# Kernel optimization log

Hardware: AMD Instinct MI355X
Metric: run time of the kernel (lower is better)

## Reference

```python
import jax, jax.numpy as jnp
import numpy as np

NUM_GRAPHS = 512  # static number of segments (graphs in the batch)
EPS = 1e-05


def setup_inputs() -> dict:
    key = jax.random.key(0)
    k1, k2 = jax.random.split(key)
    N, C = 500000, 128
    x = jax.random.normal(k1, (N, C), dtype=jnp.float32)
    batch = jnp.sort(jax.random.randint(k2, (N,), 0, NUM_GRAPHS)).astype(jnp.int64)
    weight = jnp.ones((C,), dtype=jnp.float32)
    bias = jnp.zeros((C,), dtype=jnp.float32)
    return {"x": x, "batch": batch, "weight": weight, "bias": bias}


def reference(x, batch, weight, bias):
    # Per-graph mean/var over nodes (dim=0 within each graph), per channel.
    seg = batch.astype(jnp.int32)
    counts = jax.ops.segment_sum(jnp.ones((x.shape[0],), x.dtype), seg,
                                 num_segments=NUM_GRAPHS)  # [B]
    counts = jnp.maximum(counts, 1.0)[:, None]             # guard empty graphs
    sums = jax.ops.segment_sum(x, seg, num_segments=NUM_GRAPHS)          # [B, C]
    sqsums = jax.ops.segment_sum(x * x, seg, num_segments=NUM_GRAPHS)    # [B, C]
    mean = sums / counts                                   # [B, C]
    var = sqsums / counts - mean * mean                    # biased (unbiased=False)
    inv_std = jax.lax.rsqrt(var + EPS)
    out = (x - mean[seg]) * inv_std[seg]                   # gather per node
    return out * weight + bias
```

## Files before the change

### kernel.cpp

```cpp
#include <hip/hip_runtime.h>

#define NUM_GRAPHS 512
#define EPS 1e-5f
#define CHN 128
#define CHN4 32

__device__ __forceinline__ int lower_bound_i(const int* __restrict__ b, int n, int val) {
    int l = 0, r = n;
    while (l < r) {
        int m = (l + r) >> 1;
        if (b[m] < val) l = m + 1; else r = m;
    }
    return l;
}

__global__ __launch_bounds__(256) void gln_kernel(
    const float* __restrict__ x,
    const int* __restrict__ batch,
    const float* __restrict__ weight,
    const float* __restrict__ bias,
    float* __restrict__ out,
    int N)
{
    const int s   = blockIdx.x;
    const int tid = threadIdx.x;
    const int q   = tid & 31;
    const int g   = tid >> 5;

    const int lo = lower_bound_i(batch, N, s);
    const int hi = lower_bound_i(batch, N, s + 1);

    const float4* __restrict__ x4 = (const float4*)x;
    float4*       __restrict__ o4 = (float4*)out;

    float4 sum = make_float4(0.f, 0.f, 0.f, 0.f);
    float4 sq  = make_float4(0.f, 0.f, 0.f, 0.f);
    for (int row = lo + g; row < hi; row += 8) {
        float4 v = x4[(size_t)row * CHN4 + q];
        sum.x += v.x; sum.y += v.y; sum.z += v.z; sum.w += v.w;
        sq.x  += v.x * v.x; sq.y += v.y * v.y; sq.z += v.z * v.z; sq.w += v.w * v.w;
    }

    __shared__ float4 s_sum[256];
    __shared__ float4 s_sq[256];
    s_sum[tid] = sum; s_sq[tid] = sq;
    __syncthreads();

    for (int off = 128; off >= 32; off >>= 1) {
        if (tid < off) {
            float4 a = s_sum[tid], b = s_sum[tid + off];
            a.x += b.x; a.y += b.y; a.z += b.z; a.w += b.w;
            s_sum[tid] = a;
            float4 c = s_sq[tid], d = s_sq[tid + off];
            c.x += d.x; c.y += d.y; c.z += d.z; c.w += d.w;
            s_sq[tid] = c;
        }
        __syncthreads();
    }

    if (tid < 32) {
        float cnt = (float)(hi - lo);
        float inv_cnt = 1.f / fmaxf(cnt, 1.f);
        float4 m = s_sum[tid];
        m.x *= inv_cnt; m.y *= inv_cnt; m.z *= inv_cnt; m.w *= inv_cnt;
        float4 e2 = s_sq[tid];
        float4 inv;
        inv.x = rsqrtf(e2.x * inv_cnt - m.x * m.x + EPS);
        inv.y = rsqrtf(e2.y * inv_cnt - m.y * m.y + EPS);
        inv.z = rsqrtf(e2.z * inv_cnt - m.z * m.z + EPS);
        inv.w = rsqrtf(e2.w * inv_cnt - m.w * m.w + EPS);
        s_sum[tid] = m;
        s_sq[tid]  = inv;
    }
    __syncthreads();

    const float4 m4 = s_sum[q];
    const float4 i4 = s_sq[q];
    const float4 w4 = ((const float4*)weight)[q];
    const float4 b4 = ((const float4*)bias)[q];

    for (int row = lo + g; row < hi; row += 8) {
        size_t idx = (size_t)row * CHN4 + q;
        float4 v = x4[idx];
        float4 r;
        r.x = (v.x - m4.x) * i4.x * w4.x + b4.x;
        r.y = (v.y - m4.y) * i4.y * w4.y + b4.y;
        r.z = (v.z - m4.z) * i4.z * w4.z + b4.z;
        r.w = (v.w - m4.w) * i4.w * w4.w + b4.w;
        o4[idx] = r;
    }
}

extern "C" void kernel_launch(void* const* d_in, const int* in_sizes, int n_in,
                              void* d_out, int out_size, void* d_ws, size_t ws_size,
                              hipStream_t stream) {
    const float* x      = (const float*)d_in[0];
    const int*   batch  = (const int*)d_in[1];
    const float* weight = (const float*)d_in[2];
    const float* bias   = (const float*)d_in[3];
    float*       out    = (float*)d_out;
    const int N = in_sizes[0] / CHN;

    gln_kernel<<<NUM_GRAPHS, 256, 0, stream>>>(x, batch, weight, bias, out, N);
}
```

Baseline: 495.5 us.

## Split graph norm into partial-stats, finalize, and flat normalize kernels

Replaces the single kernel, which used one block per graph, with three kernels. The first computes partial sums over eight portions per graph, so there are 4096 blocks instead of 512. A small finalize kernel folds weight and bias into a per-graph scale and shift, and a flat grid-stride kernel normalizes with one FMA per element. This is meant to fix the low occupancy of 512 blocks on a large GPU. In exchange it adds two kernel launches, a workspace round trip, and a per-element lookup of batch and stats.

```diff
diff --git a/kernel.cpp b/kernel.cpp
--- a/kernel.cpp
+++ b/kernel.cpp
@@ -4,6 +4,7 @@
 #define EPS 1e-5f
 #define CHN 128
 #define CHN4 32
+#define PORTIONS 8
 
 __device__ __forceinline__ int lower_bound_i(const int* __restrict__ b, int n, int val) {
     int l = 0, r = n;
@@ -14,15 +15,14 @@
     return l;
 }
 
-__global__ __launch_bounds__(256) void gln_kernel(
+__global__ __launch_bounds__(256) void gln_stage1(
     const float* __restrict__ x,
     const int* __restrict__ batch,
-    const float* __restrict__ weight,
-    const float* __restrict__ bias,
-    float* __restrict__ out,
+    float* __restrict__ ws_part,
     int N)
 {
-    const int s   = blockIdx.x;
+    const int s   = blockIdx.x >> 3;
+    const int p   = blockIdx.x & (PORTIONS - 1);
     const int tid = threadIdx.x;
     const int q   = tid & 31;
     const int g   = tid >> 5;
@@ -31,11 +31,10 @@
     const int hi = lower_bound_i(batch, N, s + 1);
 
     const float4* __restrict__ x4 = (const float4*)x;
-    float4*       __restrict__ o4 = (float4*)out;
 
     float4 sum = make_float4(0.f, 0.f, 0.f, 0.f);
     float4 sq  = make_float4(0.f, 0.f, 0.f, 0.f);
-    for (int row = lo + g; row < hi; row += 8) {
+    for (int row = lo + p * 8 + g; row < hi; row += 64) {
         float4 v = x4[(size_t)row * CHN4 + q];
         sum.x += v.x; sum.y += v.y; sum.z += v.z; sum.w += v.w;
         sq.x  += v.x * v.x; sq.y += v.y * v.y; sq.z += v.z * v.z; sq.w += v.w * v.w;
@@ -58,36 +57,69 @@
         __syncthreads();
     }
 
-    if (tid < 32) {
-        float cnt = (float)(hi - lo);
-        float inv_cnt = 1.f / fmaxf(cnt, 1.f);
-        float4 m = s_sum[tid];
-        m.x *= inv_cnt; m.y *= inv_cnt; m.z *= inv_cnt; m.w *= inv_cnt;
-        float4 e2 = s_sq[tid];
-        float4 inv;
-        inv.x = rsqrtf(e2.x * inv_cnt - m.x * m.x + EPS);
-        inv.y = rsqrtf(e2.y * inv_cnt - m.y * m.y + EPS);
-        inv.z = rsqrtf(e2.z * inv_cnt - m.z * m.z + EPS);
-        inv.w = rsqrtf(e2.w * inv_cnt - m.w * m.w + EPS);
-        s_sum[tid] = m;
-        s_sq[tid]  = inv;
+    float4* out4 = (float4*)ws_part + (size_t)blockIdx.x * 64;
+    if (tid < 32) out4[tid] = s_sum[tid];
+    else if (tid < 64) out4[tid] = s_sq[tid - 32];
+}
+
+__global__ __launch_bounds__(128) void gln_finalize(
+    const float* __restrict__ ws_part,
+    const int* __restrict__ batch,
+    const float* __restrict__ weight,
+    const float* __restrict__ bias,
+    float* __restrict__ ws_stats,
+    int N)
+{
+    const int s = blockIdx.x;
+    const int c = threadIdx.x;
+
+    const int lo = lower_bound_i(batch, N, s);
+    const int hi = lower_bound_i(batch, N, s + 1);
+
+    float sum = 0.f, sq = 0.f;
+    const float* base = ws_part + (size_t)s * PORTIONS * 256;
+    #pragma unroll
+    for (int p = 0; p < PORTIONS; ++p) {
+        sum += base[p * 256 + c];
+        sq  += base[p * 256 + 128 + c];
     }
-    __syncthreads();
+    float inv_cnt = 1.f / fmaxf((float)(hi - lo), 1.f);
+    float mean = sum * inv_cnt;
+    float inv_std = rsqrtf(sq * inv_cnt - mean * mean + EPS);
+    float scale = inv_std * weight[c];
+    float shift = bias[c] - mean * scale;
+    ws_stats[(size_t)s * 256 + c]       = scale;
+    ws_stats[(size_t)s * 256 + 128 + c] = shift;
+}
 
-    const float4 m4 = s_sum[q];
-    const float4 i4 = s_sq[q];
-    const float4 w4 = ((const float4*)weight)[q];
-    const float4 b4 = ((const float4*)bias)[q];
+__global__ __launch_bounds__(256) void gln_normalize(
+    const float* __restrict__ x,
+    const int* __restrict__ batch,
+    const float* __restrict__ ws_stats,
+    float* __restrict__ out,
+    int N)
+{
+    const float4* __restrict__ x4 = (const float4*)x;
+    const float4* __restrict__ st4 = (const float4*)ws_stats;
+    float4* __restrict__ o4 = (float4*)out;
 
-    for (int row = lo + g; row < hi; row += 8) {
-        size_t idx = (size_t)row * CHN4 + q;
-        float4 v = x4[idx];
+    const size_t total = (size_t)N * CHN4;
+    size_t e = (size_t)blockIdx.x * blockDim.x + threadIdx.x;
+    const size_t stride = (size_t)gridDim.x * blockDim.x;
+
+    for (; e < total; e += stride) {
+        int row = (int)(e >> 5);
+        int q   = (int)(e & 31);
+        int seg = batch[row];
+        float4 sc = st4[(size_t)seg * 64 + q];
+        float4 sh = st4[(size_t)seg * 64 + 32 + q];
+        float4 v  = x4[e];
         float4 r;
-        r.x = (v.x - m4.x) * i4.x * w4.x + b4.x;
-        r.y = (v.y - m4.y) * i4.y * w4.y + b4.y;
-        r.z = (v.z - m4.z) * i4.z * w4.z + b4.z;
-        r.w = (v.w - m4.w) * i4.w * w4.w + b4.w;
-        o4[idx] = r;
+        r.x = fmaf(v.x, sc.x, sh.x);
+        r.y = fmaf(v.y, sc.y, sh.y);
+        r.z = fmaf(v.z, sc.z, sh.z);
+        r.w = fmaf(v.w, sc.w, sh.w);
+        o4[e] = r;
     }
 }
 
@@ -101,5 +133,13 @@
     float*       out    = (float*)d_out;
     const int N = in_sizes[0] / CHN;
 
-    gln_kernel<<<NUM_GRAPHS, 256, 0, stream>>>(x, batch, weight, bias, out, N);
+    float* ws_part  = (float*)d_ws;
+    float* ws_stats = ws_part + (size_t)NUM_GRAPHS * PORTIONS * 256;
+
+    gln_stage1<<<NUM_GRAPHS * PORTIONS, 256, 0, stream>>>(x, batch, ws_part, N);
+    gln_finalize<<<NUM_GRAPHS, 128, 0, stream>>>(ws_part, batch, weight, bias, ws_stats, N);
+
+    const size_t total4 = (size_t)N * CHN4;
+    int nblocks = (int)((total4 + 256 * 4 - 1) / (256 * 4));
+    gln_normalize<<<nblocks, 256, 0, stream>>>(x, batch, ws_stats, out, N);
 }
```

After: 488.4 us. Within noise of the previous version (-1.4%).
